# Kernel tuning notes

Measured on AMD Instinct MI355X. Metric: run time of the kernel, lower is better.

Reference implementation:

```python
import jax, jax.numpy as jnp
import numpy as np

N, E = 20000, 320000
IN_DIM, EDGE_DIM, HID = 64, 16, 64
# (in_c, heads, channels, out_c) per layer; last layer heads=1, concat=False
DIMS = [(64, 4, 64, 256), (256, 4, 64, 256), (256, 1, 64, 64)]


def _ln(x, g, b):
    m = x.mean(-1, keepdims=True)
    v = x.var(-1, keepdims=True)
    return (x - m) / jnp.sqrt(v + 1e-5) * g + b


def _gatv2(x, ei, ea, Wl, bl, Wr, br, We, att, bc, concat):
    # PyG GATv2Conv, eval mode (no dropout), add_self_loops=True, fill_value='mean'
    n = x.shape[0]
    H, C = att.shape
    ar = jnp.arange(n, dtype=ei.dtype)
    src = jnp.concatenate([ei[0], ar])
    dst = jnp.concatenate([ei[1], ar])
    ea_f = jnp.concatenate([ea, jnp.broadcast_to(ea.mean(0), (n, ea.shape[1]))], 0)
    xl = (x @ Wl + bl).reshape(n, H, C)   # source transform
    xr = (x @ Wr + br).reshape(n, H, C)   # target transform
    ee = (ea_f @ We).reshape(-1, H, C)    # edge transform (no bias in PyG)
    e = jax.nn.leaky_relu(xl[src] + xr[dst] + ee, 0.2)       # [E+N, H, C]
    score = jnp.einsum('ehc,hc->eh', e, att)                 # [E+N, H]
    mx = jax.ops.segment_max(score, dst, num_segments=n)
    a = jnp.exp(score - mx[dst])
    a = a / (jax.ops.segment_sum(a, dst, num_segments=n)[dst] + 1e-16)
    out = jax.ops.segment_sum(a[:, :, None] * xl[src], dst, num_segments=n)  # [N,H,C]
    out = out.reshape(n, H * C) if concat else out.mean(1)
    return out + bc


def _forward(x, eis, eas, Wp, bp, gp, bep, layers):
    h = jax.nn.gelu(_ln(x @ Wp + bp, gp, bep), approximate=False)
    for i in range(3):
        Wl, bl, Wr, br, We, att, bc, g, be, Wsk, bsk = layers[i]
        res = h @ Wsk + bsk
        h = _gatv2(h, eis[i], eas[i], Wl, bl, Wr, br, We, att, bc, i < 2)
        h = jax.nn.gelu(_ln(h, g, be), approximate=False) + res
    return h


def setup_inputs() -> dict:
    key = jax.random.key(0)
    ks = iter(jax.random.split(key, 64))
    rn = lambda shape, s=0.05: jax.random.normal(next(ks), shape, jnp.float32) * s
    d = {'x': jax.random.normal(next(ks), (N, IN_DIM), jnp.float32)}
    for i in range(3):
        d['ei%d' % i] = jax.random.randint(next(ks), (2, E), 0, N, jnp.int32)
        d['ea%d' % i] = jax.random.normal(next(ks), (E, EDGE_DIM), jnp.float32)
    d['Wp'] = rn((IN_DIM, HID)); d['bp'] = jnp.zeros(HID)
    d['gp'] = jnp.ones(HID); d['bep'] = jnp.zeros(HID)
    for i, (ic, H, C, oc) in enumerate(DIMS):
        hc = H * C
        d['Wl%d' % i] = rn((ic, hc)); d['bl%d' % i] = jnp.zeros(hc)
        d['Wr%d' % i] = rn((ic, hc)); d['br%d' % i] = jnp.zeros(hc)
        d['We%d' % i] = rn((EDGE_DIM, hc))
        d['att%d' % i] = rn((H, C), 0.1)
        d['bc%d' % i] = jnp.zeros(hc if i < 2 else C)
        d['g%d' % i] = jnp.ones(oc); d['be%d' % i] = jnp.zeros(oc)
        d['Wsk%d' % i] = rn((ic, oc)); d['bsk%d' % i] = jnp.zeros(oc)
    return d


def reference(x, ei0, ea0, ei1, ea1, ei2, ea2, Wp, bp, gp, bep,
              Wl0, bl0, Wr0, br0, We0, att0, bc0, g0, be0, Wsk0, bsk0,
              Wl1, bl1, Wr1, br1, We1, att1, bc1, g1, be1, Wsk1, bsk1,
              Wl2, bl2, Wr2, br2, We2, att2, bc2, g2, be2, Wsk2, bsk2):
    layers = [
        (Wl0, bl0, Wr0, br0, We0, att0, bc0, g0, be0, Wsk0, bsk0),
        (Wl1, bl1, Wr1, br1, We1, att1, bc1, g1, be1, Wsk1, bsk1),
        (Wl2, bl2, Wr2, br2, We2, att2, bc2, g2, be2, Wsk2, bsk2),
    ]
    return _forward(x, (ei0, ei1, ei2), (ea0, ea1, ea2), Wp, bp, gp, bep, layers)
```

## Files before the change

kernel.cpp:

```cpp
#include <hip/hip_runtime.h>
#include <hip/hip_bf16.h>
#include <math.h>

#define NV 20000
#define NE 320000
#define CSR_PAD 16

typedef __attribute__((ext_vector_type(8))) short bf16x8;
typedef __attribute__((ext_vector_type(4))) float f32x4;
typedef __attribute__((ext_vector_type(2))) _Float16 h2;

static __device__ __forceinline__ ushort f2b(float f) {
  __hip_bfloat16 h = __float2bfloat16(f);
  return *reinterpret_cast<ushort*>(&h);
}
static __device__ __forceinline__ float b2f(ushort u) {
  union { ushort s[2]; float f; } c;
  c.s[0] = 0; c.s[1] = u;
  return c.f;
}
static __device__ __forceinline__ ushort f2h(float f) {
  _Float16 h = (_Float16)f;
  return *reinterpret_cast<ushort*>(&h);
}
static __device__ __forceinline__ float blo(unsigned u) { return __uint_as_float(u << 16); }
static __device__ __forceinline__ float bhi(unsigned u) { return __uint_as_float(u & 0xffff0000u); }
static __device__ __forceinline__ h2 u2h2(unsigned u) {
  union { unsigned v; h2 h; } c; c.v = u; return c.h;
}

static __device__ __forceinline__ float wave_sum64(float x) {
  x += __int_as_float(__builtin_amdgcn_update_dpp(0, __float_as_int(x), 0x111, 0xF, 0xF, true));
  x += __int_as_float(__builtin_amdgcn_update_dpp(0, __float_as_int(x), 0x112, 0xF, 0xF, true));
  x += __int_as_float(__builtin_amdgcn_update_dpp(0, __float_as_int(x), 0x114, 0xF, 0xF, true));
  x += __int_as_float(__builtin_amdgcn_update_dpp(0, __float_as_int(x), 0x118, 0xF, 0xF, true));
  x += __int_as_float(__builtin_amdgcn_update_dpp(0, __float_as_int(x), 0x142, 0xA, 0xF, true));
  x += __int_as_float(__builtin_amdgcn_update_dpp(0, __float_as_int(x), 0x143, 0xC, 0xF, true));
  return __int_as_float(__builtin_amdgcn_readlane(__float_as_int(x), 63));
}

static __device__ __forceinline__ float sum16(float x) {
  x += __int_as_float(__builtin_amdgcn_update_dpp(0, __float_as_int(x), 0x121, 0xF, 0xF, true));
  x += __int_as_float(__builtin_amdgcn_update_dpp(0, __float_as_int(x), 0x122, 0xF, 0xF, true));
  x += __int_as_float(__builtin_amdgcn_update_dpp(0, __float_as_int(x), 0x124, 0xF, 0xF, true));
  x += __int_as_float(__builtin_amdgcn_update_dpp(0, __float_as_int(x), 0x128, 0xF, 0xF, true));
  return x;
}

static __device__ __forceinline__ float dot16h_i(const uint4* __restrict__ E,
                                                 const h2* __restrict__ Wch,
                                                 float s) {
#if __has_builtin(__builtin_amdgcn_fdot2)
  const h2* e = (const h2*)E;
#pragma unroll
  for (int j = 0; j < 8; ++j) s = __builtin_amdgcn_fdot2(e[j], Wch[j], s, false);
  return s;
#else
  const unsigned* u = (const unsigned*)E;
#pragma unroll
  for (int j = 0; j < 8; ++j) {
    union { unsigned v; h2 h; } cv; cv.v = u[j];
    s = fmaf((float)cv.h[0], (float)Wch[j][0], s);
    s = fmaf((float)cv.h[1], (float)Wch[j][1], s);
  }
  return s;
#endif
}

struct HArgs {
  const int* ei[3]; int* counts;
  const float* ea[3]; float* easum[3];
};

__global__ __launch_bounds__(256) void hist_kernel(HArgs a) {
  const int t = threadIdx.x, b = (int)blockIdx.x;
  if (b < 3750) {
    int gi = b * 256 + t;
    int l = gi / NE, i = gi - l * NE;
    atomicAdd(&a.counts[(size_t)l * (NV + 1) + a.ei[l][NE + i]], 1);
  } else {
    const int cb = b - 3750;
    const int l = cb >> 8, blk = cb & 255;
    const float4* ea4 = (const float4*)a.ea[l];
    const int cg = t & 3;
    int r = blk * 64 + (t >> 2);
    const int rstride = 256 * 64;
    float4 s = make_float4(0.f, 0.f, 0.f, 0.f);
    for (; r < NE; r += rstride) {
      float4 v = ea4[(size_t)r * 4 + cg];
      s.x += v.x; s.y += v.y; s.z += v.z; s.w += v.w;
    }
    __shared__ float4 red4[256];
    red4[t] = s;
    __syncthreads();
    if (t < 4) {
      float4 tot = make_float4(0.f, 0.f, 0.f, 0.f);
      for (int j = t; j < 256; j += 4) {
        float4 v = red4[j];
        tot.x += v.x; tot.y += v.y; tot.z += v.z; tot.w += v.w;
      }
      atomicAdd(&a.easum[l][t * 4 + 0], tot.x);
      atomicAdd(&a.easum[l][t * 4 + 1], tot.y);
      atomicAdd(&a.easum[l][t * 4 + 2], tot.z);
      atomicAdd(&a.easum[l][t * 4 + 3], tot.w);
    }
  }
}

struct CJob { const float* src; ushort* dst; int K, M; };
struct K2Args {
  const int* counts; int* offs; int* cursor;
  CJob jobs[9];
  unsigned* csr[3]; ushort* eab[3];
  const float *x, *Wp, *bp, *gp, *bep;
  ushort* h0;
  const float* easum;
  const float* We[3];
  unsigned* wchx[3];
  float* esfO[3];
};

__global__ __launch_bounds__(1024) void scan_proj_kernel(K2Args a) {
  const int b = blockIdx.x, t = threadIdx.x;
  if (b < 3) {
    const int* counts = a.counts + b * (NV + 1);
    int* offs = a.offs + b * (NV + 1);
    int* cursor = a.cursor + b * NV;
    __shared__ int ws[16];
    __shared__ int wexcl[17];
    const int lane = t & 63, wid = t >> 6;
    const int base = t * 20;
    int v[20];
    int tot = 0;
#pragma unroll
    for (int j = 0; j < 20; ++j) {
      int i = base + j;
      v[j] = (i < NV) ? counts[i] : 0;
      tot += v[j];
    }
    int x = tot;
#pragma unroll
    for (int o = 1; o < 64; o <<= 1) {
      int yy = __shfl_up(x, o, 64);
      if (lane >= o) x += yy;
    }
    if (lane == 63) ws[wid] = x;
    __syncthreads();
    if (t == 0) {
      int r = 0;
#pragma unroll
      for (int j = 0; j < 16; ++j) { wexcl[j] = r; r += ws[j]; }
      wexcl[16] = r;
    }
    __syncthreads();
    int run = wexcl[wid] + (x - tot);
#pragma unroll
    for (int j = 0; j < 20; ++j) {
      int i = base + j;
      if (i < NV) { offs[i] = run; cursor[i] = run; }
      run += v[j];
    }
    if (t == 0) offs[NV] = wexcl[16];
  } else if (b < 19) {
    if (b == 3 && t < 3 * CSR_PAD) {
      int l = t >> 4, p = t & 15;
      a.csr[l][NE + p] = 0u;
      uint4 z = make_uint4(0, 0, 0, 0);
      *(uint4*)(a.eab[l] + (size_t)(NE + p) * 16) = z;
      *(uint4*)(a.eab[l] + (size_t)(NE + p) * 16 + 8) = z;
    }
#pragma unroll
    for (int j = 0; j < 9; ++j) {
      CJob jb = a.jobs[j];
      const int total = jb.M * jb.K;
      for (int i = (b - 3) * 1024 + t; i < total; i += 16 * 1024) {
        int m = i / jb.K, k = i - m * jb.K;
        jb.dst[i] = f2b(jb.src[(size_t)k * jb.M + m]);
      }
    }
  } else if (b < 19 + NV / 16) {
    const int wid = t >> 6, lane = t & 63;
    const int row = (b - 19) * 16 + wid;
    float xv = a.x[(size_t)row * 64 + lane];
    float acc = a.bp[lane];
#pragma unroll
    for (int k = 0; k < 64; ++k) {
      float v = __shfl(xv, k, 64);
      acc = fmaf(v, a.Wp[k * 64 + lane], acc);
    }
    float s1 = wave_sum64(acc), s2 = wave_sum64(acc * acc);
    float mean = s1 * (1.0f / 64.0f);
    float var  = s2 * (1.0f / 64.0f) - mean * mean;
    float yv = (acc - mean) * rsqrtf(var + 1e-5f) * a.gp[lane] + a.bep[lane];
    float gel = 0.5f * yv * (1.0f + erff(yv * 0.70710678118654752f));
    a.h0[(size_t)row * 64 + lane] = f2b(gel);
  } else {
    for (int i = t; i < 4608; i += 1024) {
      int l, e;
      if (i < 2048)      { l = 0; e = i; }
      else if (i < 4096) { l = 1; e = i - 2048; }
      else               { l = 2; e = i - 4096; }
      const int hcl = (l == 2) ? 64 : 256;
      int k8 = e / hcl, c = e - k8 * hcl;
      const float* We = a.We[l];
      a.wchx[l][e] = (unsigned)f2h(We[(2 * k8) * hcl + c]) |
                     ((unsigned)f2h(We[(2 * k8 + 1) * hcl + c]) << 16);
    }
    for (int i = t; i < 576; i += 1024) {
      int l, c;
      if (i < 256)      { l = 0; c = i; }
      else if (i < 512) { l = 1; c = i - 256; }
      else              { l = 2; c = i - 512; }
      const int hcl = (l == 2) ? 64 : 256;
      const float* We = a.We[l];
      const float* es = a.easum + l * 16;
      float s = 0.f;
#pragma unroll
      for (int k8 = 0; k8 < 8; ++k8) {
        s = fmaf(es[2 * k8], We[(2 * k8) * hcl + c], s);
        s = fmaf(es[2 * k8 + 1], We[(2 * k8 + 1) * hcl + c], s);
      }
      a.esfO[l][c] = s * (1.0f / (float)NE);
    }
  }
}

struct K3Args {
  const ushort *A, *WT;
  const float *b0, *b1, *b2;
  ushort *O0, *O1; float* O2;
  int K, M1, M2, Mtot, NT;
  const int* ei[3]; const float* ea[3];
  int* cursor;
  unsigned* csr[3]; ushort* eab[3]; int HC[3];
};

__global__ __launch_bounds__(256) void mega_kernel(K3Args a) {
  __shared__ ushort As[128][40];
  __shared__ ushort Bs[64][40];
  const int t = threadIdx.x;
  const int b = (int)blockIdx.x;
  if (b < a.NT) {
    const int wave = t >> 6, lane = t & 63;
    const int mcols = a.Mtot >> 6;
    const int col0 = (b % mcols) * 64, row0 = (b / mcols) * 128;
    const int m_ = lane & 15, q = lane >> 4;
    f32x4 acc[2][4];
#pragma unroll
    for (int i = 0; i < 2; ++i)
#pragma unroll
      for (int j = 0; j < 4; ++j) acc[i][j] = (f32x4){0.f, 0.f, 0.f, 0.f};
    const int ar = t >> 1, ac = (t & 1) * 16;
    const int br = t >> 2, bcol = (t & 3) * 8;
    const ushort* Ap = a.A + (size_t)(row0 + ar) * a.K + ac;
    const ushort* Bp = a.WT + (size_t)(col0 + br) * a.K + bcol;
    const bool a_ok = (row0 + ar) < NV;
    for (int k0 = 0; k0 < a.K; k0 += 32) {
      uint4 av0 = make_uint4(0, 0, 0, 0), av1 = make_uint4(0, 0, 0, 0);
      if (a_ok) { av0 = *(const uint4*)(Ap + k0); av1 = *(const uint4*)(Ap + k0 + 8); }
      uint4 bv = *(const uint4*)(Bp + k0);
      *(uint4*)&As[ar][ac] = av0;
      *(uint4*)&As[ar][ac + 8] = av1;
      *(uint4*)&Bs[br][bcol] = bv;
      __syncthreads();
      bf16x8 a0 = *(const bf16x8*)&As[wave * 32 + m_][q * 8];
      bf16x8 a1 = *(const bf16x8*)&As[wave * 32 + 16 + m_][q * 8];
#pragma unroll
      for (int cf = 0; cf < 4; ++cf) {
        bf16x8 bfr = *(const bf16x8*)&Bs[cf * 16 + m_][q * 8];
        acc[0][cf] = __builtin_amdgcn_mfma_f32_16x16x32_bf16(a0, bfr, acc[0][cf], 0, 0, 0);
        acc[1][cf] = __builtin_amdgcn_mfma_f32_16x16x32_bf16(a1, bfr, acc[1][cf], 0, 0, 0);
      }
      __syncthreads();
    }
    const float* bias; int base, mode, Wd;
    if (col0 < a.M1)      { bias = a.b0; base = 0;    mode = 0; Wd = a.M1; }
    else if (col0 < a.M2) { bias = a.b1; base = a.M1; mode = 1; Wd = a.M2 - a.M1; }
    else                  { bias = a.b2; base = a.M2; mode = 2; Wd = a.Mtot - a.M2; }
#pragma unroll
    for (int rf = 0; rf < 2; ++rf) {
#pragma unroll
      for (int cf = 0; cf < 4; ++cf) {
        int col = col0 + cf * 16 + m_ - base;
        float bb = bias[col];
#pragma unroll
        for (int r = 0; r < 4; ++r) {
          int row = row0 + wave * 32 + rf * 16 + q * 4 + r;
          if (row < NV) {
            float v = acc[rf][cf][r] + bb;
            if (mode == 0)      a.O0[(size_t)row * Wd + col] = f2b(v);
            else if (mode == 1) a.O1[(size_t)row * Wd + col] = f2b(v);
            else                a.O2[(size_t)row * Wd + col] = v;
          }
        }
      }
    }
  } else {
    int gi = (b - a.NT) * 256 + t;
    int l = gi / NE, i = gi - l * NE;
    int dst = a.ei[l][NE + i], src = a.ei[l][i];
    int pos = atomicAdd(&a.cursor[(size_t)l * NV + dst], 1);
    a.csr[l][pos] = (unsigned)(src * a.HC[l]);
    const float4* er = (const float4*)(a.ea[l] + (size_t)i * 16);
    float4 q0 = er[0], q1 = er[1], q2 = er[2], q3 = er[3];
    uint4 w0, w1;
    w0.x = (unsigned)f2h(q0.x) | ((unsigned)f2h(q0.y) << 16);
    w0.y = (unsigned)f2h(q0.z) | ((unsigned)f2h(q0.w) << 16);
    w0.z = (unsigned)f2h(q1.x) | ((unsigned)f2h(q1.y) << 16);
    w0.w = (unsigned)f2h(q1.z) | ((unsigned)f2h(q1.w) << 16);
    w1.x = (unsigned)f2h(q2.x) | ((unsigned)f2h(q2.y) << 16);
    w1.y = (unsigned)f2h(q2.z) | ((unsigned)f2h(q2.w) << 16);
    w1.z = (unsigned)f2h(q3.x) | ((unsigned)f2h(q3.y) << 16);
    w1.w = (unsigned)f2h(q3.z) | ((unsigned)f2h(q3.w) << 16);
    *(uint4*)(a.eab[l] + (size_t)pos * 16) = w0;
    *(uint4*)(a.eab[l] + (size_t)pos * 16 + 8) = w1;
  }
}

__global__ __launch_bounds__(256) void gemm_fused(
    const ushort* __restrict__ A, const ushort* __restrict__ WT,
    const float* __restrict__ b0, const float* __restrict__ b1,
    const float* __restrict__ b2,
    ushort* __restrict__ O0, ushort* __restrict__ O1, float* __restrict__ O2,
    int N, int K, int M1, int M2, int Mtot)
{
  __shared__ ushort As[128][40];
  __shared__ ushort Bs[64][40];
  const int t = threadIdx.x, wave = t >> 6, lane = t & 63;
  const int row0 = blockIdx.y * 128, col0 = blockIdx.x * 64;
  const int m_ = lane & 15, q = lane >> 4;
  f32x4 acc[2][4];
#pragma unroll
  for (int i = 0; i < 2; ++i)
#pragma unroll
    for (int j = 0; j < 4; ++j) acc[i][j] = (f32x4){0.f, 0.f, 0.f, 0.f};
  const int ar = t >> 1, ac = (t & 1) * 16;
  const int br = t >> 2, bcol = (t & 3) * 8;
  const ushort* Ap = A + (size_t)(row0 + ar) * K + ac;
  const ushort* Bp = WT + (size_t)(col0 + br) * K + bcol;
  const bool a_ok = (row0 + ar) < N;
  for (int k0 = 0; k0 < K; k0 += 32) {
    uint4 av0 = make_uint4(0, 0, 0, 0), av1 = make_uint4(0, 0, 0, 0);
    if (a_ok) { av0 = *(const uint4*)(Ap + k0); av1 = *(const uint4*)(Ap + k0 + 8); }
    uint4 bv = *(const uint4*)(Bp + k0);
    *(uint4*)&As[ar][ac] = av0;
    *(uint4*)&As[ar][ac + 8] = av1;
    *(uint4*)&Bs[br][bcol] = bv;
    __syncthreads();
    bf16x8 a0 = *(const bf16x8*)&As[wave * 32 + m_][q * 8];
    bf16x8 a1 = *(const bf16x8*)&As[wave * 32 + 16 + m_][q * 8];
#pragma unroll
    for (int cf = 0; cf < 4; ++cf) {
      bf16x8 bfr = *(const bf16x8*)&Bs[cf * 16 + m_][q * 8];
      acc[0][cf] = __builtin_amdgcn_mfma_f32_16x16x32_bf16(a0, bfr, acc[0][cf], 0, 0, 0);
      acc[1][cf] = __builtin_amdgcn_mfma_f32_16x16x32_bf16(a1, bfr, acc[1][cf], 0, 0, 0);
    }
    __syncthreads();
  }
  const float* bias; int base, mode, Wd;
  if (col0 < M1)      { bias = b0; base = 0;  mode = 0; Wd = M1; }
  else if (col0 < M2) { bias = b1; base = M1; mode = 1; Wd = M2 - M1; }
  else                { bias = b2; base = M2; mode = 2; Wd = Mtot - M2; }
#pragma unroll
  for (int rf = 0; rf < 2; ++rf) {
#pragma unroll
    for (int cf = 0; cf < 4; ++cf) {
      int col = col0 + cf * 16 + m_ - base;
      float bb = bias[col];
#pragma unroll
      for (int r = 0; r < 4; ++r) {
        int row = row0 + wave * 32 + rf * 16 + q * 4 + r;
        if (row < N) {
          float v = acc[rf][cf][r] + bb;
          if (mode == 0)      O0[(size_t)row * Wd + col] = f2b(v);
          else if (mode == 1) O1[(size_t)row * Wd + col] = f2b(v);
          else                O2[(size_t)row * Wd + col] = v;
        }
      }
    }
  }
}

__global__ __launch_bounds__(256) void agg4_kernel(
    const ushort* __restrict__ eab, const unsigned* __restrict__ wchx,
    const float* __restrict__ esf,
    const ushort* __restrict__ xl, const ushort* __restrict__ xr,
    const float* __restrict__ att, const float* __restrict__ bc,
    const float* __restrict__ g, const float* __restrict__ be,
    const float* __restrict__ res,
    const int* __restrict__ offs, const unsigned* __restrict__ csr,
    ushort* __restrict__ houtb)
{
  const int t = threadIdx.x, lane = t & 63, wave = t >> 6;
  const int n = blockIdx.x * 4 + wave;
  const int cb = 4 * lane;
  const size_t rowb = (size_t)n * 256 + cb;
  const float L2E = 1.4426950408889634f;

  float4 atv = *(const float4*)(att + cb);
  float at[4] = {atv.x * L2E, atv.y * L2E, atv.z * L2E, atv.w * L2E};

  h2 Wch[4][8];
#pragma unroll
  for (int k8 = 0; k8 < 8; ++k8) {
    uint4 wv = *(const uint4*)(wchx + k8 * 256 + cb);
    Wch[0][k8] = u2h2(wv.x); Wch[1][k8] = u2h2(wv.y);
    Wch[2][k8] = u2h2(wv.z); Wch[3][k8] = u2h2(wv.w);
  }
  float4 esfv = *(const float4*)(esf + cb);
  const float* esfp = &esfv.x;

  uint2 qr = *(const uint2*)(xr + rowb);
  float xrv[4] = {blo(qr.x), bhi(qr.x), blo(qr.y), bhi(qr.y)};
  uint2 qn = *(const uint2*)(xl + rowb);
  float xln[4] = {blo(qn.x), bhi(qn.x), blo(qn.y), bhi(qn.y)};

  float p = 0.f;
#pragma unroll
  for (int j = 0; j < 4; ++j) {
    float v = xln[j] + xrv[j] + esfp[j];
    v = v > 0.f ? v : 0.2f * v;
    p = fmaf(v, at[j], p);
  }
  float wself = exp2f(sum16(p));
  float acc[4];
#pragma unroll
  for (int j = 0; j < 4; ++j) acc[j] = wself * xln[j];
  float denom = wself;

  const int beg = __builtin_amdgcn_readfirstlane(offs[n]);
  const int end = __builtin_amdgcn_readfirstlane(offs[n + 1]);

  unsigned CA[2];
  uint4 EA[2][2];
  uint2 XL[2], XN1[2];
  {
    unsigned C0[2], C1[2];
#pragma unroll
    for (int k = 0; k < 2; ++k) C0[k] = csr[beg + k];
#pragma unroll
    for (int k = 0; k < 2; ++k) C1[k] = csr[beg + 2 + k];
#pragma unroll
    for (int k = 0; k < 2; ++k) CA[k] = csr[beg + 4 + k];
#pragma unroll
    for (int k = 0; k < 2; ++k) {
      const uint4* ep = (const uint4*)(eab + (size_t)(beg + k) * 16);
      EA[k][0] = ep[0]; EA[k][1] = ep[1];
    }
#pragma unroll
    for (int k = 0; k < 2; ++k)
      XL[k] = *(const uint2*)(xl + __builtin_amdgcn_readfirstlane(C0[k]) + cb);
#pragma unroll
    for (int k = 0; k < 2; ++k)
      XN1[k] = *(const uint2*)(xl + __builtin_amdgcn_readfirstlane(C1[k]) + cb);
  }

  for (int idx = beg; idx < end; idx += 2) {
    unsigned CB[2];
#pragma unroll
    for (int k = 0; k < 2; ++k) CB[k] = csr[idx + 6 + k];
    uint4 EB[2][2];
#pragma unroll
    for (int k = 0; k < 2; ++k) {
      const uint4* ep = (const uint4*)(eab + (size_t)(idx + 2 + k) * 16);
      EB[k][0] = ep[0]; EB[k][1] = ep[1];
    }
    uint2 XN2[2];
#pragma unroll
    for (int k = 0; k < 2; ++k)
      XN2[k] = *(const uint2*)(xl + __builtin_amdgcn_readfirstlane(CA[k]) + cb);

#pragma unroll
    for (int k = 0; k < 2; ++k) {
      float xf[4] = {blo(XL[k].x), bhi(XL[k].x), blo(XL[k].y), bhi(XL[k].y)};
      float pp = 0.f;
#pragma unroll
      for (int j = 0; j < 4; ++j) {
        float v = dot16h_i(EA[k], Wch[j], xf[j] + xrv[j]);
        v = v > 0.f ? v : 0.2f * v;
        pp = fmaf(v, at[j], pp);
      }
      float S = sum16(pp);
      float w = (idx + k < end) ? exp2f(S) : 0.f;
#pragma unroll
      for (int j = 0; j < 4; ++j) acc[j] = fmaf(w, xf[j], acc[j]);
      denom += w;
    }
#pragma unroll
    for (int k = 0; k < 2; ++k) {
      EA[k][0] = EB[k][0]; EA[k][1] = EB[k][1];
      XL[k] = XN1[k]; XN1[k] = XN2[k]; CA[k] = CB[k];
    }
  }

  const float inv = 1.0f / (denom + 1e-16f);
  float4 bcv = *(const float4*)(bc + cb);
  float out[4];
  out[0] = acc[0] * inv + bcv.x; out[1] = acc[1] * inv + bcv.y;
  out[2] = acc[2] * inv + bcv.z; out[3] = acc[3] * inv + bcv.w;

  float so1 = out[0] + out[1] + out[2] + out[3];
  float so2 = out[0] * out[0] + out[1] * out[1] + out[2] * out[2] + out[3] * out[3];
  float s1 = wave_sum64(so1), s2 = wave_sum64(so2);
  float mean = s1 * (1.0f / 256.0f);
  float var  = s2 * (1.0f / 256.0f) - mean * mean;
  float rstd = rsqrtf(var + 1e-5f);
  float4 gv = *(const float4*)(g + cb);
  float4 bev = *(const float4*)(be + cb);
  float4 rv = *(const float4*)(res + rowb);
  const float* gp = &gv.x; const float* bep = &bev.x; const float* rp = &rv.x;
  ushort ob[4];
#pragma unroll
  for (int j = 0; j < 4; ++j) {
    float y = (out[j] - mean) * rstd * gp[j] + bep[j];
    float gel = 0.5f * y * (1.0f + erff(y * 0.70710678118654752f));
    ob[j] = f2b(gel + rp[j]);
  }
  uint2 ov;
  ov.x = (unsigned)ob[0] | ((unsigned)ob[1] << 16);
  ov.y = (unsigned)ob[2] | ((unsigned)ob[3] << 16);
  *(uint2*)(houtb + rowb) = ov;
}

__global__ __launch_bounds__(256, 4) void agg1_kernel(
    const ushort* __restrict__ eab, const unsigned* __restrict__ wchx,
    const float* __restrict__ esf,
    const ushort* __restrict__ xl, const ushort* __restrict__ xr,
    const float* __restrict__ att, const float* __restrict__ bc,
    const float* __restrict__ g, const float* __restrict__ be,
    const float* __restrict__ res,
    const int* __restrict__ offs, const unsigned* __restrict__ csr,
    float* __restrict__ houtf)
{
  const int HC = 64;
  const int t = threadIdx.x, lane = t & 63, wave = t >> 6;
  const int n = blockIdx.x * 4 + wave;
  const int c = lane;

  const float xr_t = b2f(xr[(size_t)n * HC + c]);
  const float att_t = att[c] * 1.4426950408889634f;
  h2 Wch[8];
#pragma unroll
  for (int k8 = 0; k8 < 8; ++k8) Wch[k8] = u2h2(wchx[k8 * 64 + c]);
  const float eself = esf[c];
  const float xln = b2f(xl[(size_t)n * HC + c]);

  float vs = xln + xr_t + eself;
  vs = vs > 0.f ? vs : 0.2f * vs;
  const float wself = exp2f(wave_sum64(vs * att_t));
  float acc = wself * xln, denom = wself;

  const int beg = __builtin_amdgcn_readfirstlane(offs[n]);
  const int end = __builtin_amdgcn_readfirstlane(offs[n + 1]);

  unsigned CA[4];
  uint4 EA[4][2];
  float XL[4], XN1[4];
  {
    unsigned C0[4], C1[4];
#pragma unroll
    for (int k = 0; k < 4; ++k) C0[k] = csr[beg + k];
#pragma unroll
    for (int k = 0; k < 4; ++k) C1[k] = csr[beg + 4 + k];
#pragma unroll
    for (int k = 0; k < 4; ++k) CA[k] = csr[beg + 8 + k];
#pragma unroll
    for (int k = 0; k < 4; ++k) {
      const uint4* ep = (const uint4*)(eab + (size_t)(beg + k) * 16);
      EA[k][0] = ep[0]; EA[k][1] = ep[1];
    }
#pragma unroll
    for (int k = 0; k < 4; ++k)
      XL[k] = b2f(xl[__builtin_amdgcn_readfirstlane(C0[k]) + c]);
#pragma unroll
    for (int k = 0; k < 4; ++k)
      XN1[k] = b2f(xl[__builtin_amdgcn_readfirstlane(C1[k]) + c]);
  }

  for (int idx = beg; idx < end; idx += 4) {
    unsigned CB[4];
#pragma unroll
    for (int k = 0; k < 4; ++k) CB[k] = csr[idx + 12 + k];
    uint4 EB[4][2];
#pragma unroll
    for (int k = 0; k < 4; ++k) {
      const uint4* ep = (const uint4*)(eab + (size_t)(idx + 4 + k) * 16);
      EB[k][0] = ep[0]; EB[k][1] = ep[1];
    }
    float XN2[4];
#pragma unroll
    for (int k = 0; k < 4; ++k)
      XN2[k] = b2f(xl[__builtin_amdgcn_readfirstlane(CA[k]) + c]);

    float wv[4];
#pragma unroll
    for (int k = 0; k < 4; ++k) {
      float v = dot16h_i(EA[k], Wch, XL[k] + xr_t);
      v = v > 0.f ? v : 0.2f * v;
      float S = wave_sum64(v * att_t);
      wv[k] = (idx + k < end) ? exp2f(S) : 0.f;
    }
#pragma unroll
    for (int k = 0; k < 4; ++k) { acc = fmaf(wv[k], XL[k], acc); denom += wv[k]; }
#pragma unroll
    for (int k = 0; k < 4; ++k) {
      EA[k][0] = EB[k][0]; EA[k][1] = EB[k][1];
      XL[k] = XN1[k]; XN1[k] = XN2[k]; CA[k] = CB[k];
    }
  }

  float out = acc / (denom + 1e-16f) + bc[c];
  float s1 = wave_sum64(out), s2 = wave_sum64(out * out);
  float mean = s1 / (float)HC;
  float var  = s2 / (float)HC - mean * mean;
  float y = (out - mean) * rsqrtf(var + 1e-5f) * g[c] + be[c];
  float gel = 0.5f * y * (1.0f + erff(y * 0.70710678118654752f));
  houtf[(size_t)n * HC + c] = gel + res[(size_t)n * HC + c];
}

extern "C" void kernel_launch(void* const* d_in, const int* in_sizes, int n_in,
                              void* d_out, int out_size, void* d_ws, size_t ws_size,
                              hipStream_t stream)
{
  auto in = [&](int i) { return (const float*)d_in[i]; };

  const int ic[3] = {64, 256, 256}, hc[3] = {256, 256, 64}, oc[3] = {256, 256, 64};
  const int CSRN = NE + CSR_PAD;

  char* w = (char*)d_ws;
  size_t off = 0;
  auto alloc = [&](size_t bytes) { void* p = w + off; off = (off + bytes + 511) & ~(size_t)511; return p; };
  ushort* B1   = (ushort*)alloc((size_t)NV * 256 * 2);
  ushort* B2   = (ushort*)alloc((size_t)NV * 256 * 2);
  float*  B3   = (float*)alloc((size_t)NV * 256 * 4);
  ushort* h0bf = (ushort*)alloc((size_t)NV * 64 * 2);
  ushort* h1bf = (ushort*)alloc((size_t)NV * 256 * 2);
  ushort* h2bf = (ushort*)alloc((size_t)NV * 256 * 2);
  ushort* Wcat[3];
  for (int i = 0; i < 3; ++i)
    Wcat[i] = (ushort*)alloc((size_t)(2 * hc[i] + oc[i]) * ic[i] * 2);
  float*    easumA  = (float*)alloc(3 * 64);
  int*      countsA = (int*)alloc((size_t)3 * (NV + 1) * 4);
  int*      offsA   = (int*)alloc((size_t)3 * (NV + 1) * 4);
  int*      cursorA = (int*)alloc((size_t)3 * NV * 4);
  unsigned* csrA    = (unsigned*)alloc((size_t)3 * CSRN * 4);
  ushort*   eabA    = (ushort*)alloc((size_t)3 * CSRN * 16 * 2);
  unsigned* wchxA   = (unsigned*)alloc((size_t)4608 * 4);
  float*    esfA    = (float*)alloc((size_t)576 * 4);

  hipMemsetAsync(easumA, 0, 512 + (size_t)3 * (NV + 1) * 4, stream);

  HArgs ha;
  for (int i = 0; i < 3; ++i) {
    ha.ei[i] = (const int*)d_in[1 + 2 * i];
    ha.ea[i] = in(2 + 2 * i);
    ha.easum[i] = easumA + i * 16;
  }
  ha.counts = countsA;
  hist_kernel<<<3750 + 768, 256, 0, stream>>>(ha);

  K2Args k2;
  k2.counts = countsA; k2.offs = offsA; k2.cursor = cursorA;
  for (int i = 0; i < 3; ++i) {
    k2.jobs[i * 3 + 0] = {in(11 + 11 * i), Wcat[i],                             ic[i], hc[i]};
    k2.jobs[i * 3 + 1] = {in(13 + 11 * i), Wcat[i] + (size_t)hc[i] * ic[i],     ic[i], hc[i]};
    k2.jobs[i * 3 + 2] = {in(20 + 11 * i), Wcat[i] + (size_t)2 * hc[i] * ic[i], ic[i], oc[i]};
    k2.csr[i] = csrA + (size_t)i * CSRN;
    k2.eab[i] = eabA + (size_t)i * CSRN * 16;
    k2.We[i] = in(15 + 11 * i);
  }
  k2.x = in(0); k2.Wp = in(7); k2.bp = in(8); k2.gp = in(9); k2.bep = in(10);
  k2.h0 = h0bf;
  k2.easum = easumA;
  k2.wchx[0] = wchxA; k2.wchx[1] = wchxA + 2048; k2.wchx[2] = wchxA + 4096;
  k2.esfO[0] = esfA; k2.esfO[1] = esfA + 256; k2.esfO[2] = esfA + 512;
  scan_proj_kernel<<<19 + NV / 16 + 1, 1024, 0, stream>>>(k2);

  K3Args ga;
  ga.A = h0bf; ga.WT = Wcat[0];
  ga.b0 = in(12); ga.b1 = in(14); ga.b2 = in(21);
  ga.O0 = B1; ga.O1 = B2; ga.O2 = B3;
  ga.K = 64; ga.M1 = 256; ga.M2 = 512; ga.Mtot = 768;
  ga.NT = (768 / 64) * ((NV + 127) / 128);
  for (int i = 0; i < 3; ++i) {
    ga.ei[i] = (const int*)d_in[1 + 2 * i];
    ga.ea[i] = in(2 + 2 * i);
    ga.csr[i] = csrA + (size_t)i * CSRN;
    ga.eab[i] = eabA + (size_t)i * CSRN * 16;
    ga.HC[i] = hc[i];
  }
  ga.cursor = cursorA;
  mega_kernel<<<ga.NT + 3750, 256, 0, stream>>>(ga);

  agg4_kernel<<<NV / 4, 256, 0, stream>>>(
      eabA + 0, wchxA, esfA, B1, B2, in(16), in(17), in(18), in(19),
      B3, offsA, csrA, h1bf);

  gemm_fused<<<dim3(768 / 64, (NV + 127) / 128), 256, 0, stream>>>(
      h1bf, Wcat[1], in(23), in(25), in(32), B1, B2, B3, NV, 256, 256, 512, 768);

  agg4_kernel<<<NV / 4, 256, 0, stream>>>(
      eabA + (size_t)CSRN * 16, wchxA + 2048, esfA + 256, B1, B2, in(27), in(28),
      in(29), in(30), B3, offsA + (NV + 1), csrA + (size_t)CSRN, h2bf);

  gemm_fused<<<dim3(192 / 64, (NV + 127) / 128), 256, 0, stream>>>(
      h2bf, Wcat[2], in(34), in(36), in(43), B1, B2, B3, NV, 256, 64, 128, 192);

  agg1_kernel<<<NV / 4, 256, 0, stream>>>(
      eabA + (size_t)2 * CSRN * 16, wchxA + 4096, esfA + 512, B1, B2, in(38), in(39),
      in(40), in(41), B3, offsA + 2 * (NV + 1), csrA + (size_t)2 * CSRN,
      (float*)d_out);
}
```

Measured before the change: 524.4 us.

## Replace global atomic degree histogram with per-block LDS histograms merged in scan

Splits the combined histogram/colsum kernel in two. Degree counting now builds 16 private shared-memory histograms per layer with vectorized int4 index loads, writes them out as replicas, and the scan kernel sums the replicas. This is meant to remove contended global atomics and the memset of the counts array. In exchange it adds an extra kernel launch, an 80KB LDS footprint per block that limits occupancy to 48 blocks total, and 16x more count reads in the scan.

```diff
diff --git a/kernel.cpp b/kernel.cpp
--- a/kernel.cpp
+++ b/kernel.cpp
@@ -5,6 +5,7 @@
 #define NV 20000
 #define NE 320000
 #define CSR_PAD 16
+#define NREP 16
 
 typedef __attribute__((ext_vector_type(8))) short bf16x8;
 typedef __attribute__((ext_vector_type(4))) float f32x4;
@@ -67,43 +68,55 @@
 #endif
 }
 
-struct HArgs {
-  const int* ei[3]; int* counts;
-  const float* ea[3]; float* easum[3];
-};
-
-__global__ __launch_bounds__(256) void hist_kernel(HArgs a) {
-  const int t = threadIdx.x, b = (int)blockIdx.x;
-  if (b < 3750) {
-    int gi = b * 256 + t;
-    int l = gi / NE, i = gi - l * NE;
-    atomicAdd(&a.counts[(size_t)l * (NV + 1) + a.ei[l][NE + i]], 1);
-  } else {
-    const int cb = b - 3750;
-    const int l = cb >> 8, blk = cb & 255;
-    const float4* ea4 = (const float4*)a.ea[l];
-    const int cg = t & 3;
-    int r = blk * 64 + (t >> 2);
-    const int rstride = 256 * 64;
-    float4 s = make_float4(0.f, 0.f, 0.f, 0.f);
-    for (; r < NE; r += rstride) {
-      float4 v = ea4[(size_t)r * 4 + cg];
-      s.x += v.x; s.y += v.y; s.z += v.z; s.w += v.w;
-    }
-    __shared__ float4 red4[256];
-    red4[t] = s;
-    __syncthreads();
-    if (t < 4) {
-      float4 tot = make_float4(0.f, 0.f, 0.f, 0.f);
-      for (int j = t; j < 256; j += 4) {
-        float4 v = red4[j];
-        tot.x += v.x; tot.y += v.y; tot.z += v.z; tot.w += v.w;
-      }
-      atomicAdd(&a.easum[l][t * 4 + 0], tot.x);
-      atomicAdd(&a.easum[l][t * 4 + 1], tot.y);
-      atomicAdd(&a.easum[l][t * 4 + 2], tot.z);
-      atomicAdd(&a.easum[l][t * 4 + 3], tot.w);
-    }
+struct LHArgs { const int* ei[3]; int* counts; };
+
+__global__ __launch_bounds__(256) void lhist_kernel(LHArgs a) {
+  __shared__ int lh[NV + 1];
+  const int t = threadIdx.x;
+  const int l = blockIdx.x >> 4, r = blockIdx.x & 15;
+  for (int i = t; i < NV + 1; i += 256) lh[i] = 0;
+  __syncthreads();
+  const int4* d4 = (const int4*)(a.ei[l] + NE);
+  const int q0 = r * (NE / NREP / 4), q1 = q0 + NE / NREP / 4;
+  for (int q = q0 + t; q < q1; q += 256) {
+    int4 d = d4[q];
+    atomicAdd(&lh[d.x], 1);
+    atomicAdd(&lh[d.y], 1);
+    atomicAdd(&lh[d.z], 1);
+    atomicAdd(&lh[d.w], 1);
+  }
+  __syncthreads();
+  int* out = a.counts + (size_t)(l * NREP + r) * (NV + 1);
+  for (int i = t; i < NV + 1; i += 256) out[i] = lh[i];
+}
+
+struct ColArgs { const float* ea[3]; float* easum[3]; };
+
+__global__ __launch_bounds__(256) void colsum_kernel(ColArgs a) {
+  const int t = threadIdx.x, cb = (int)blockIdx.x;
+  const int l = cb >> 8, blk = cb & 255;
+  const float4* ea4 = (const float4*)a.ea[l];
+  const int cg = t & 3;
+  int r = blk * 64 + (t >> 2);
+  const int rstride = 256 * 64;
+  float4 s = make_float4(0.f, 0.f, 0.f, 0.f);
+  for (; r < NE; r += rstride) {
+    float4 v = ea4[(size_t)r * 4 + cg];
+    s.x += v.x; s.y += v.y; s.z += v.z; s.w += v.w;
+  }
+  __shared__ float4 red4[256];
+  red4[t] = s;
+  __syncthreads();
+  if (t < 4) {
+    float4 tot = make_float4(0.f, 0.f, 0.f, 0.f);
+    for (int j = t; j < 256; j += 4) {
+      float4 v = red4[j];
+      tot.x += v.x; tot.y += v.y; tot.z += v.z; tot.w += v.w;
+    }
+    atomicAdd(&a.easum[l][t * 4 + 0], tot.x);
+    atomicAdd(&a.easum[l][t * 4 + 1], tot.y);
+    atomicAdd(&a.easum[l][t * 4 + 2], tot.z);
+    atomicAdd(&a.easum[l][t * 4 + 3], tot.w);
   }
 }
 
@@ -123,7 +136,7 @@
 __global__ __launch_bounds__(1024) void scan_proj_kernel(K2Args a) {
   const int b = blockIdx.x, t = threadIdx.x;
   if (b < 3) {
-    const int* counts = a.counts + b * (NV + 1);
+    const int* counts = a.counts + (size_t)b * NREP * (NV + 1);
     int* offs = a.offs + b * (NV + 1);
     int* cursor = a.cursor + b * NV;
     __shared__ int ws[16];
@@ -135,8 +148,13 @@
 #pragma unroll
     for (int j = 0; j < 20; ++j) {
       int i = base + j;
-      v[j] = (i < NV) ? counts[i] : 0;
-      tot += v[j];
+      int c = 0;
+      if (i < NV) {
+#pragma unroll
+        for (int rr = 0; rr < NREP; ++rr) c += counts[(size_t)rr * (NV + 1) + i];
+      }
+      v[j] = c;
+      tot += c;
     }
     int x = tot;
 #pragma unroll
@@ -640,7 +658,7 @@
   for (int i = 0; i < 3; ++i)
     Wcat[i] = (ushort*)alloc((size_t)(2 * hc[i] + oc[i]) * ic[i] * 2);
   float*    easumA  = (float*)alloc(3 * 64);
-  int*      countsA = (int*)alloc((size_t)3 * (NV + 1) * 4);
+  int*      countsA = (int*)alloc((size_t)3 * NREP * (NV + 1) * 4);
   int*      offsA   = (int*)alloc((size_t)3 * (NV + 1) * 4);
   int*      cursorA = (int*)alloc((size_t)3 * NV * 4);
   unsigned* csrA    = (unsigned*)alloc((size_t)3 * CSRN * 4);
@@ -648,16 +666,19 @@
   unsigned* wchxA   = (unsigned*)alloc((size_t)4608 * 4);
   float*    esfA    = (float*)alloc((size_t)576 * 4);
 
-  hipMemsetAsync(easumA, 0, 512 + (size_t)3 * (NV + 1) * 4, stream);
-
-  HArgs ha;
+  hipMemsetAsync(easumA, 0, 512, stream);
+
+  LHArgs lh;
+  for (int i = 0; i < 3; ++i) lh.ei[i] = (const int*)d_in[1 + 2 * i];
+  lh.counts = countsA;
+  lhist_kernel<<<3 * NREP, 256, 0, stream>>>(lh);
+
+  ColArgs ca;
   for (int i = 0; i < 3; ++i) {
-    ha.ei[i] = (const int*)d_in[1 + 2 * i];
-    ha.ea[i] = in(2 + 2 * i);
-    ha.easum[i] = easumA + i * 16;
-  }
-  ha.counts = countsA;
-  hist_kernel<<<3750 + 768, 256, 0, stream>>>(ha);
+    ca.ea[i] = in(2 + 2 * i);
+    ca.easum[i] = easumA + i * 16;
+  }
+  colsum_kernel<<<768, 256, 0, stream>>>(ca);
 
   K2Args k2;
   k2.counts = countsA; k2.offs = offsA; k2.cursor = cursorA;
```

Measured after the change: 590.5 us. +12.6%, slower.
